# Performance work log

Measured on AMD Instinct MI355X. Metric: run time of the kernel, lower is better.

Reference implementation:

```python
import jax, jax.numpy as jnp
import numpy as np
from jax import lax

B_J0 = 0.01
BETA = 1.8
GAMMA = 0.5
LENS = 0.5
SCALE = 6.0
HIGHT = 0.15


def _gaussian(x, mu, sigma):
    return jnp.exp(-((x - mu) ** 2) / (2.0 * sigma ** 2)) / (jnp.sqrt(2.0 * jnp.pi) * sigma)


@jax.custom_vjp
def spike_fn(v):
    return (v > 0).astype(v.dtype)


def _spike_fwd(v):
    return spike_fn(v), v


def _spike_bwd(v, g):
    temp = (_gaussian(v, 0.0, LENS) * (1.0 + HIGHT)
            - _gaussian(v, LENS, SCALE * LENS) * HIGHT
            - _gaussian(v, -LENS, SCALE * LENS) * HIGHT)
    return (g * temp * GAMMA,)


spike_fn.defvjp(_spike_fwd, _spike_bwd)


def setup_inputs() -> dict:
    key = jax.random.key(0)
    ks = jax.random.split(key, 8)
    S, B, D, H = 1024, 2048, 2, 128
    x = jax.random.normal(ks[0], (S, B, D), dtype=jnp.float32)
    y = jax.random.normal(ks[1], (B,), dtype=jnp.float32)
    z = jnp.zeros((B, H), dtype=jnp.float32)

    def lin_init(k, out_f, in_f):
        bound = 1.0 / np.sqrt(in_f)
        return jax.random.uniform(k, (out_f, in_f), jnp.float32, -bound, bound)

    W1x = lin_init(ks[2], H, D + H)
    WtauM = lin_init(ks[3], H, 2 * H)
    WtauAdp = lin_init(ks[4], H, 2 * H)
    # readout uses xavier_normal_
    Wlin = jax.random.normal(ks[5], (1, H), jnp.float32) * np.sqrt(2.0 / (1 + H))
    return {
        'x': x, 'y': y,
        'h0_mem': z, 'h0_spk': z, 'h0_b': z,
        'W1x': W1x, 'b1x': jnp.zeros((H,), jnp.float32),
        'WtauM': WtauM, 'btauM': jnp.zeros((H,), jnp.float32),
        'WtauAdp': WtauAdp, 'btauAdp': jnp.zeros((H,), jnp.float32),
        'Wlin': Wlin, 'blin': jnp.zeros((1,), jnp.float32),
    }


def reference(x, y, h0_mem, h0_spk, h0_b, W1x, b1x, WtauM, btauM, WtauAdp, btauAdp, Wlin, blin):
    def step(carry, x_t):
        mem, spk, bb = carry
        dense = jnp.concatenate([x_t, spk], axis=-1) @ W1x.T + b1x          # [B,H]
        tauM = jax.nn.sigmoid(jnp.concatenate([dense, mem], axis=-1) @ WtauM.T + btauM)
        tauA = jax.nn.sigmoid(jnp.concatenate([dense, bb], axis=-1) @ WtauAdp.T + btauAdp)
        bb = tauA * bb + (1.0 - tauA) * spk
        Bth = B_J0 + BETA * bb
        mem = mem * tauM + (1.0 - tauM) * dense - Bth * spk
        spk = spike_fn(mem - Bth)
        return (mem, spk, bb), None

    (mem, spk, bb), _ = lax.scan(step, (h0_mem, h0_spk, h0_b), x)
    out = (mem @ Wlin.T + blin)[:, 0]                                       # [B]
    loss = jnp.mean((out - y) ** 2)
    return loss
```

## Files before the change

### kernel.cpp

```cpp
#include <hip/hip_runtime.h>
#include <math.h>

#define S_LEN 1024
#define BATCH 2048
#define MTILE 8
#define HID   128
#define NBLK  (BATCH / MTILE)
#define INV2048 (1.0f / 2048.0f)

#define H_M1H 0
#define H_M1L 20480
#define H_MSH 40960
#define H_MSL 61440
#define H_ASH 81920
#define H_ASL 102400
#define H_WMH 122880
#define H_WML 139264
#define H_WBH 155648
#define H_WBL 172032
#define OFF_PART_F 94208

typedef _Float16 half8 __attribute__((ext_vector_type(8)));
typedef _Float16 half4 __attribute__((ext_vector_type(4)));
typedef float floatx4 __attribute__((ext_vector_type(4)));

#define MFMA(a, b, c) __builtin_amdgcn_mfma_f32_16x16x32_f16((a), (b), (c), 0, 0, 0)

__device__ __forceinline__ void put_hl(_Float16* ws, int hiBase, int loBase,
                                       int idx, float v) {
  _Float16 hi = (_Float16)v;
  ws[hiBase + idx] = hi;
  ws[loBase + idx] = (_Float16)((v - (float)hi) * 2048.0f);
}

__device__ __forceinline__ float dpp_xor8(float v) {
  int sw = __builtin_amdgcn_update_dpp(0, __float_as_int(v),
                                       0x128 , 0xF, 0xF, true);
  return __int_as_float(sw);
}

__global__ __launch_bounds__(192) void prep(
    const float* __restrict__ W1x, const float* __restrict__ b1x,
    const float* __restrict__ WtauM, const float* __restrict__ btauM,
    const float* __restrict__ WtauAdp, const float* __restrict__ btauAdp,
    _Float16* __restrict__ ws) {
  const int h = blockIdx.x, k = threadIdx.x;
  if (k >= 160) return;
  if (k < 128) {
    float w1 = W1x[h * 130 + 2 + k];
    float s1 = 0.f, s2 = 0.f;
    for (int d = 0; d < 128; ++d) {
      float wd = W1x[d * 130 + 2 + k];
      s1 += WtauM[h * 256 + d] * wd;
      s2 += WtauAdp[h * 256 + d] * wd;
    }
    put_hl(ws, H_M1H, H_M1L, h * 160 + k, w1);
    put_hl(ws, H_MSH, H_MSL, h * 160 + k, s1);
    put_hl(ws, H_ASH, H_ASL, h * 160 + k, s2);
    put_hl(ws, H_WMH, H_WML, h * 128 + k, WtauM[h * 256 + 128 + k]);
    put_hl(ws, H_WBH, H_WBL, h * 128 + k, WtauAdp[h * 256 + 128 + k]);
  } else if (k < 131) {
    const int col = k - 128;
    float m1v = (col == 0) ? b1x[h] : W1x[h * 130 + (col - 1)];
    float sm = 0.f, sa = 0.f;
    for (int d = 0; d < 128; ++d) {
      float cv = (col == 0) ? b1x[d] : W1x[d * 130 + (col - 1)];
      sm += WtauM[h * 256 + d] * cv;
      sa += WtauAdp[h * 256 + d] * cv;
    }
    if (col == 0) { sm += btauM[h]; sa += btauAdp[h]; }
    put_hl(ws, H_M1H, H_M1L, h * 160 + k, m1v);
    put_hl(ws, H_MSH, H_MSL, h * 160 + k, sm);
    put_hl(ws, H_ASH, H_ASL, h * 160 + k, sa);
  } else {
    put_hl(ws, H_M1H, H_M1L, h * 160 + k, 0.f);
    put_hl(ws, H_MSH, H_MSL, h * 160 + k, 0.f);
    put_hl(ws, H_ASH, H_ASL, h * 160 + k, 0.f);
  }
}

struct SLds {
  _Float16 spk[2][4][256];
  _Float16 zero16[8];
  _Float16 mem[2][4][512];
  _Float16 bbp[2][4][512];
  float red[8][8];
  float red2[8];
};

__global__ __launch_bounds__(512, 2) void snn_main(
    const float* __restrict__ x, const float* __restrict__ y,
    const float* __restrict__ h0m, const float* __restrict__ h0s,
    const float* __restrict__ h0b,
    const float* __restrict__ Wlin, const float* __restrict__ blin,
    const _Float16* __restrict__ W, float* __restrict__ wsout) {
  __shared__ SLds L;

  const int tid  = threadIdx.x;
  const int w    = tid >> 6;
  const int lane = tid & 63;
  const int c    = lane & 15;
  const int q    = lane >> 4;
  const int bbase = blockIdx.x * MTILE;
  const bool act = (c < 8);

  half8 m1h[5], m1l[5], msh[5], msl[5], ash[5], asl[5];
  half8 wmh[4], wml[4], wbh[4], wbl[4];
  {
    const int hA = w * 16 + c;
#pragma unroll
    for (int f = 0; f < 5; ++f) {
      const int o = hA * 160 + f * 32 + q * 8;
      m1h[f] = *(const half8*)&W[H_M1H + o];
      m1l[f] = *(const half8*)&W[H_M1L + o];
      msh[f] = *(const half8*)&W[H_MSH + o];
      msl[f] = *(const half8*)&W[H_MSL + o];
      ash[f] = *(const half8*)&W[H_ASH + o];
      asl[f] = *(const half8*)&W[H_ASL + o];
    }
#pragma unroll
    for (int f = 0; f < 4; ++f) {
      const int o = hA * 128 + f * 32 + q * 8;
      wmh[f] = *(const half8*)&W[H_WMH + o];
      wml[f] = *(const half8*)&W[H_WML + o];
      wbh[f] = *(const half8*)&W[H_WBH + o];
      wbl[f] = *(const half8*)&W[H_WBL + o];
    }
  }

  if (tid == 0) {
    *(half8*)&L.zero16[0] = half8{0, 0, 0, 0, 0, 0, 0, 0};
  }

  float memv[4], spk[4], bb[4];
#pragma unroll
  for (int r = 0; r < 4; ++r) { memv[r] = 0.f; spk[r] = 0.f; bb[r] = 0.f; }
  if (act) {
#pragma unroll
    for (int r = 0; r < 4; ++r) {
      const int gi = (bbase + c) * HID + w * 16 + q * 4 + r;
      memv[r] = h0m[gi]; spk[r] = h0s[gi]; bb[r] = h0b[gi];
    }
  }

  const int fW  = w >> 1;
  const int qp  = (w & 1) * 2 + (q >> 1);
  const int wiH = (qp * 16 + c) * 8 + (q & 1) * 4;
  const int wiL = wiH + 64;
  const int wiS = (qp * 8 + c) * 8 + (q & 1) * 4;
  const int ri  = lane * 8;
  const _Float16* spkB0 = act ? &L.spk[0][0][(q * 8 + c) * 8] : L.zero16;
  const _Float16* spkB1 = act ? &L.spk[1][0][(q * 8 + c) * 8] : L.zero16;
  const int spkStep = act ? 256 : 0;

  if (act) {
    half4 ps, mh4, ml4, bh4, bl4;
#pragma unroll
    for (int r = 0; r < 4; ++r) {
      ps[r] = (_Float16)spk[r];
      float v = memv[r]; _Float16 hi = (_Float16)v;
      mh4[r] = hi; ml4[r] = (_Float16)((v - (float)hi) * 2048.0f);
      v = bb[r]; hi = (_Float16)v;
      bh4[r] = hi; bl4[r] = (_Float16)((v - (float)hi) * 2048.0f);
    }
    *(half4*)&L.spk[0][fW][wiS] = ps;
    *(half4*)&L.mem[0][fW][wiH] = mh4; *(half4*)&L.mem[0][fW][wiL] = ml4;
    *(half4*)&L.bbp[0][fW][wiH] = bh4; *(half4*)&L.bbp[0][fW][wiL] = bl4;
  }
  __syncthreads();

  const float* xb = x + (size_t)(bbase + (c & 7)) * 2;
  float2 xv = *(const float2*)xb;
  const _Float16 e0c = act ? (_Float16)1.0f : (_Float16)0.0f;

#pragma unroll 1
  for (int t = 0; t < S_LEN; ++t) {
    const int p = t & 1, pn = p ^ 1;
    const size_t tn = (t + 1 < S_LEN) ? (size_t)(t + 1) : (size_t)t;
    float2 xnx = *(const float2*)(xb + tn * (size_t)(BATCH * 2));

    half8 E;
    {
      _Float16 xh0 = (_Float16)xv.x, xh1 = (_Float16)xv.y;
      _Float16 xl0 = (_Float16)((xv.x - (float)xh0) * 2048.0f);
      _Float16 xl1 = (_Float16)((xv.y - (float)xh1) * 2048.0f);
      E = half8{e0c, act ? xh0 : xl0, act ? xh1 : xl1, 0, 0, 0, 0, 0};
    }

    const _Float16* sB = p ? spkB1 : spkB0;

    floatx4 d1 = {0.f,0.f,0.f,0.f}, d2 = {0.f,0.f,0.f,0.f};
    floatx4 m1 = {0.f,0.f,0.f,0.f}, m2 = {0.f,0.f,0.f,0.f};
    floatx4 a1 = {0.f,0.f,0.f,0.f}, a2 = {0.f,0.f,0.f,0.f};

#pragma unroll
    for (int f = 0; f < 4; ++f) {
      half8 S = *(const half8*)&sB[f * spkStep];
      half8 M = *(const half8*)&L.mem[p][f][ri];
      half8 B = *(const half8*)&L.bbp[p][f][ri];
      d1 = MFMA(m1h[f], S, d1);
      d2 = MFMA(m1l[f], S, d2);
      m1 = MFMA(msh[f], S, m1);
      m1 = MFMA(wmh[f], M, m1);
      m2 = MFMA(msl[f], S, m2);
      m2 = MFMA(wml[f], M, m2);
      a1 = MFMA(ash[f], S, a1);
      a1 = MFMA(wbh[f], B, a1);
      a2 = MFMA(asl[f], S, a2);
      a2 = MFMA(wbl[f], B, a2);
    }
    {
      d1 = MFMA(m1h[4], E, d1);
      d2 = MFMA(m1l[4], E, d2);
      m1 = MFMA(msh[4], E, m1);
      m2 = MFMA(msl[4], E, m2);
      a1 = MFMA(ash[4], E, a1);
      a2 = MFMA(asl[4], E, a2);
    }

#pragma unroll
    for (int r = 0; r < 4; ++r) {
      d2[r] += dpp_xor8(d1[r]);
      m2[r] += dpp_xor8(m1[r]);
      a2[r] += dpp_xor8(a1[r]);
    }

    half4 ps, mh4, ml4, bh4, bl4;
#pragma unroll
    for (int r = 0; r < 4; ++r) {
      float den  = d1[r] + d2[r] * INV2048;
      float preM = m1[r] + m2[r] * INV2048;
      float preA = a1[r] + a2[r] * INV2048;
      float tM = __builtin_amdgcn_rcpf(1.0f + __expf(-preM));
      float tA = __builtin_amdgcn_rcpf(1.0f + __expf(-preA));
      bb[r] = tA * bb[r] + (1.0f - tA) * spk[r];
      float Bth = 0.01f + 1.8f * bb[r];
      memv[r] = memv[r] * tM + (1.0f - tM) * den - Bth * spk[r];
      spk[r] = (memv[r] - Bth) > 0.0f ? 1.0f : 0.0f;
      ps[r] = (_Float16)spk[r];
      float v = memv[r]; _Float16 hi = (_Float16)v;
      mh4[r] = hi; ml4[r] = (_Float16)((v - (float)hi) * 2048.0f);
      v = bb[r]; hi = (_Float16)v;
      bh4[r] = hi; bl4[r] = (_Float16)((v - (float)hi) * 2048.0f);
    }
    if (act) {
      *(half4*)&L.spk[pn][fW][wiS] = ps;
      *(half4*)&L.mem[pn][fW][wiH] = mh4; *(half4*)&L.mem[pn][fW][wiL] = ml4;
      *(half4*)&L.bbp[pn][fW][wiH] = bh4; *(half4*)&L.bbp[pn][fW][wiL] = bl4;
    }
    xv = xnx;
    __syncthreads();
  }

  float part = 0.0f;
#pragma unroll
  for (int r = 0; r < 4; ++r)
    part += memv[r] * Wlin[w * 16 + q * 4 + r];
  part += __shfl_xor(part, 16);
  part += __shfl_xor(part, 32);
  if (lane < 8) L.red[w][c] = part;
  __syncthreads();
  if (tid < 8) {
    float s = 0.0f;
#pragma unroll
    for (int ww = 0; ww < 8; ++ww) s += L.red[ww][tid];
    float out = s + blin[0];
    float d = out - y[bbase + tid];
    L.red2[tid] = d * d;
  }
  __syncthreads();
  if (tid == 0) {
    float s = 0.0f;
#pragma unroll
    for (int m = 0; m < MTILE; ++m) s += L.red2[m];
    wsout[blockIdx.x] = s;
  }
}

__global__ __launch_bounds__(256) void final_reduce(const float* __restrict__ part,
                                                    float* __restrict__ out) {
  __shared__ float sh[256];
  int t = threadIdx.x;
  sh[t] = part[t];
  __syncthreads();
  for (int s = 128; s > 0; s >>= 1) {
    if (t < s) sh[t] += sh[t + s];
    __syncthreads();
  }
  if (t == 0) out[0] = sh[0] * (1.0f / (float)BATCH);
}

extern "C" void kernel_launch(void* const* d_in, const int* in_sizes, int n_in,
                              void* d_out, int out_size, void* d_ws, size_t ws_size,
                              hipStream_t stream) {
  const float* x       = (const float*)d_in[0];
  const float* y       = (const float*)d_in[1];
  const float* h0m     = (const float*)d_in[2];
  const float* h0s     = (const float*)d_in[3];
  const float* h0b     = (const float*)d_in[4];
  const float* W1x     = (const float*)d_in[5];
  const float* b1x     = (const float*)d_in[6];
  const float* WtauM   = (const float*)d_in[7];
  const float* btauM   = (const float*)d_in[8];
  const float* WtauAdp = (const float*)d_in[9];
  const float* btauAdp = (const float*)d_in[10];
  const float* Wlin    = (const float*)d_in[11];
  const float* blin    = (const float*)d_in[12];
  _Float16* wsf16 = (_Float16*)d_ws;
  float* wspart = (float*)d_ws + OFF_PART_F;

  prep<<<128, 192, 0, stream>>>(W1x, b1x, WtauM, btauM, WtauAdp, btauAdp, wsf16);
  snn_main<<<NBLK, 512, 0, stream>>>(x, y, h0m, h0s, h0b, Wlin, blin,
                                     wsf16, wspart);
  final_reduce<<<1, 256, 0, stream>>>(wspart, (float*)d_out);
}
```

Measured before the change: 1.757 ms.

## Use all 16 MFMA columns for batch rows instead of hi/lo split lanes

Doubles the batch tile per block from 8 to 16 rows so every MFMA column carries a real batch element. The fp16 hi/lo compensation moves from lane halves (combined via DPP) to separate hi and lo LDS buffers plus extra MFMA accumulators. The negative log2(e) factor is folded into the precomputed tau weights so the sigmoid uses exp2 directly. This halves the block count to 128 with one block per CU and adds two MFMAs per k-slice, trading occupancy and extra matrix work for removing wasted columns and DPP shuffles.

```diff
diff --git a/kernel.cpp b/kernel.cpp
--- a/kernel.cpp
+++ b/kernel.cpp
@@ -3,10 +3,11 @@
 
 #define S_LEN 1024
 #define BATCH 2048
-#define MTILE 8
+#define MTILE 16
 #define HID   128
 #define NBLK  (BATCH / MTILE)
 #define INV2048 (1.0f / 2048.0f)
+#define NLOG2E (-1.44269504088896341f)
 
 #define H_M1H 0
 #define H_M1L 20480
@@ -31,12 +32,6 @@
   _Float16 hi = (_Float16)v;
   ws[hiBase + idx] = hi;
   ws[loBase + idx] = (_Float16)((v - (float)hi) * 2048.0f);
-}
-
-__device__ __forceinline__ float dpp_xor8(float v) {
-  int sw = __builtin_amdgcn_update_dpp(0, __float_as_int(v),
-                                       0x128 , 0xF, 0xF, true);
-  return __int_as_float(sw);
 }
 
 __global__ __launch_bounds__(192) void prep(
@@ -55,12 +50,12 @@
       s2 += WtauAdp[h * 256 + d] * wd;
     }
     put_hl(ws, H_M1H, H_M1L, h * 160 + k, w1);
-    put_hl(ws, H_MSH, H_MSL, h * 160 + k, s1);
-    put_hl(ws, H_ASH, H_ASL, h * 160 + k, s2);
-    put_hl(ws, H_WMH, H_WML, h * 128 + k, WtauM[h * 256 + 128 + k]);
-    put_hl(ws, H_WBH, H_WBL, h * 128 + k, WtauAdp[h * 256 + 128 + k]);
-  } else if (k < 131) {
-    const int col = k - 128;
+    put_hl(ws, H_MSH, H_MSL, h * 160 + k, s1 * NLOG2E);
+    put_hl(ws, H_ASH, H_ASL, h * 160 + k, s2 * NLOG2E);
+    put_hl(ws, H_WMH, H_WML, h * 128 + k, WtauM[h * 256 + 128 + k] * NLOG2E);
+    put_hl(ws, H_WBH, H_WBL, h * 128 + k, WtauAdp[h * 256 + 128 + k] * NLOG2E);
+  } else if (k < 133) {
+    const int col = (k == 128) ? 0 : ((k == 129 || k == 131) ? 1 : 2);
     float m1v = (col == 0) ? b1x[h] : W1x[h * 130 + (col - 1)];
     float sm = 0.f, sa = 0.f;
     for (int d = 0; d < 128; ++d) {
@@ -69,26 +64,36 @@
       sa += WtauAdp[h * 256 + d] * cv;
     }
     if (col == 0) { sm += btauM[h]; sa += btauAdp[h]; }
-    put_hl(ws, H_M1H, H_M1L, h * 160 + k, m1v);
-    put_hl(ws, H_MSH, H_MSL, h * 160 + k, sm);
-    put_hl(ws, H_ASH, H_ASL, h * 160 + k, sa);
+    sm *= NLOG2E; sa *= NLOG2E;
+    const int idx = h * 160 + k;
+    if (k < 131) {
+      put_hl(ws, H_M1H, H_M1L, idx, m1v);
+      put_hl(ws, H_MSH, H_MSL, idx, sm);
+      put_hl(ws, H_ASH, H_ASL, idx, sa);
+    } else {
+      ws[H_M1H + idx] = (_Float16)0.0f; ws[H_M1L + idx] = (_Float16)m1v;
+      ws[H_MSH + idx] = (_Float16)0.0f; ws[H_MSL + idx] = (_Float16)sm;
+      ws[H_ASH + idx] = (_Float16)0.0f; ws[H_ASL + idx] = (_Float16)sa;
+    }
   } else {
-    put_hl(ws, H_M1H, H_M1L, h * 160 + k, 0.f);
-    put_hl(ws, H_MSH, H_MSL, h * 160 + k, 0.f);
-    put_hl(ws, H_ASH, H_ASL, h * 160 + k, 0.f);
+    const int idx = h * 160 + k;
+    ws[H_M1H + idx] = 0; ws[H_M1L + idx] = 0;
+    ws[H_MSH + idx] = 0; ws[H_MSL + idx] = 0;
+    ws[H_ASH + idx] = 0; ws[H_ASL + idx] = 0;
   }
 }
 
 struct SLds {
-  _Float16 spk[2][4][256];
-  _Float16 zero16[8];
-  _Float16 mem[2][4][512];
-  _Float16 bbp[2][4][512];
-  float red[8][8];
-  float red2[8];
+  _Float16 spk[2][4][512];
+  _Float16 memh[2][4][512];
+  _Float16 meml[2][4][512];
+  _Float16 bbph[2][4][512];
+  _Float16 bbpl[2][4][512];
+  float red[8][16];
+  float red2[16];
 };
 
-__global__ __launch_bounds__(512, 2) void snn_main(
+__global__ __launch_bounds__(512, 1) void snn_main(
     const float* __restrict__ x, const float* __restrict__ y,
     const float* __restrict__ h0m, const float* __restrict__ h0s,
     const float* __restrict__ h0b,
@@ -97,17 +102,16 @@
   __shared__ SLds L;
 
   const int tid  = threadIdx.x;
-  const int w    = tid >> 6;
+  const int wg   = tid >> 6;
   const int lane = tid & 63;
   const int c    = lane & 15;
   const int q    = lane >> 4;
   const int bbase = blockIdx.x * MTILE;
-  const bool act = (c < 8);
 
   half8 m1h[5], m1l[5], msh[5], msl[5], ash[5], asl[5];
   half8 wmh[4], wml[4], wbh[4], wbl[4];
   {
-    const int hA = w * 16 + c;
+    const int hA = wg * 16 + c;
 #pragma unroll
     for (int f = 0; f < 5; ++f) {
       const int o = hA * 160 + f * 32 + q * 8;
@@ -128,50 +132,44 @@
     }
   }
 
-  if (tid == 0) {
-    *(half8*)&L.zero16[0] = half8{0, 0, 0, 0, 0, 0, 0, 0};
-  }
-
-  float memv[4], spk[4], bb[4];
-#pragma unroll
-  for (int r = 0; r < 4; ++r) { memv[r] = 0.f; spk[r] = 0.f; bb[r] = 0.f; }
-  if (act) {
+  const int h0i = wg * 16 + q * 4;
+  float memv[4], spk4[4], bb[4];
+  {
+    const int gi = (bbase + c) * HID + h0i;
+    float4 tm = *(const float4*)&h0m[gi];
+    float4 ts = *(const float4*)&h0s[gi];
+    float4 tb = *(const float4*)&h0b[gi];
+    memv[0] = tm.x; memv[1] = tm.y; memv[2] = tm.z; memv[3] = tm.w;
+    spk4[0] = ts.x; spk4[1] = ts.y; spk4[2] = ts.z; spk4[3] = ts.w;
+    bb[0]   = tb.x; bb[1]   = tb.y; bb[2]   = tb.z; bb[3]   = tb.w;
+  }
+
+  const int fW = wg >> 1;
+  const int qp = (wg & 1) * 2 + (q >> 1);
+  const int wi = (qp * 16 + c) * 8 + (q & 1) * 4;
+  const int ri = lane * 8;
+
+  {
+    half4 ps, mh4, ml4, bh4, bl4;
 #pragma unroll
     for (int r = 0; r < 4; ++r) {
-      const int gi = (bbase + c) * HID + w * 16 + q * 4 + r;
-      memv[r] = h0m[gi]; spk[r] = h0s[gi]; bb[r] = h0b[gi];
-    }
-  }
-
-  const int fW  = w >> 1;
-  const int qp  = (w & 1) * 2 + (q >> 1);
-  const int wiH = (qp * 16 + c) * 8 + (q & 1) * 4;
-  const int wiL = wiH + 64;
-  const int wiS = (qp * 8 + c) * 8 + (q & 1) * 4;
-  const int ri  = lane * 8;
-  const _Float16* spkB0 = act ? &L.spk[0][0][(q * 8 + c) * 8] : L.zero16;
-  const _Float16* spkB1 = act ? &L.spk[1][0][(q * 8 + c) * 8] : L.zero16;
-  const int spkStep = act ? 256 : 0;
-
-  if (act) {
-    half4 ps, mh4, ml4, bh4, bl4;
-#pragma unroll
-    for (int r = 0; r < 4; ++r) {
-      ps[r] = (_Float16)spk[r];
+      ps[r] = (_Float16)spk4[r];
       float v = memv[r]; _Float16 hi = (_Float16)v;
       mh4[r] = hi; ml4[r] = (_Float16)((v - (float)hi) * 2048.0f);
       v = bb[r]; hi = (_Float16)v;
       bh4[r] = hi; bl4[r] = (_Float16)((v - (float)hi) * 2048.0f);
     }
-    *(half4*)&L.spk[0][fW][wiS] = ps;
-    *(half4*)&L.mem[0][fW][wiH] = mh4; *(half4*)&L.mem[0][fW][wiL] = ml4;
-    *(half4*)&L.bbp[0][fW][wiH] = bh4; *(half4*)&L.bbp[0][fW][wiL] = bl4;
+    *(half4*)&L.spk[0][fW][wi]  = ps;
+    *(half4*)&L.memh[0][fW][wi] = mh4; *(half4*)&L.meml[0][fW][wi] = ml4;
+    *(half4*)&L.bbph[0][fW][wi] = bh4; *(half4*)&L.bbpl[0][fW][wi] = bl4;
   }
   __syncthreads();
 
-  const float* xb = x + (size_t)(bbase + (c & 7)) * 2;
+  const float qm = (q == 0) ? 1.0f : 0.0f;
+  const _Float16 e0 = (q == 0) ? (_Float16)1.0f : (_Float16)0.0f;
+
+  const float* xb = x + (size_t)(bbase + c) * 2;
   float2 xv = *(const float2*)xb;
-  const _Float16 e0c = act ? (_Float16)1.0f : (_Float16)0.0f;
 
 #pragma unroll 1
   for (int t = 0; t < S_LEN; ++t) {
@@ -181,86 +179,79 @@
 
     half8 E;
     {
-      _Float16 xh0 = (_Float16)xv.x, xh1 = (_Float16)xv.y;
-      _Float16 xl0 = (_Float16)((xv.x - (float)xh0) * 2048.0f);
-      _Float16 xl1 = (_Float16)((xv.y - (float)xh1) * 2048.0f);
-      E = half8{e0c, act ? xh0 : xl0, act ? xh1 : xl1, 0, 0, 0, 0, 0};
-    }
-
-    const _Float16* sB = p ? spkB1 : spkB0;
-
-    floatx4 d1 = {0.f,0.f,0.f,0.f}, d2 = {0.f,0.f,0.f,0.f};
-    floatx4 m1 = {0.f,0.f,0.f,0.f}, m2 = {0.f,0.f,0.f,0.f};
-    floatx4 a1 = {0.f,0.f,0.f,0.f}, a2 = {0.f,0.f,0.f,0.f};
+      float xe0 = xv.x * qm, xe1 = xv.y * qm;
+      _Float16 xh0 = (_Float16)xe0, xh1 = (_Float16)xe1;
+      _Float16 xl0 = (_Float16)((xe0 - (float)xh0) * 2048.0f);
+      _Float16 xl1 = (_Float16)((xe1 - (float)xh1) * 2048.0f);
+      E = half8{e0, xh0, xh1, xl0, xl1, 0, 0, 0};
+    }
+
+    floatx4 d1 = {0,0,0,0}, d2 = {0,0,0,0};
+    floatx4 mA1 = {0,0,0,0}, mA2 = {0,0,0,0}, mA3 = {0,0,0,0};
+    floatx4 aA1 = {0,0,0,0}, aA2 = {0,0,0,0}, aA3 = {0,0,0,0};
 
 #pragma unroll
     for (int f = 0; f < 4; ++f) {
-      half8 S = *(const half8*)&sB[f * spkStep];
-      half8 M = *(const half8*)&L.mem[p][f][ri];
-      half8 B = *(const half8*)&L.bbp[p][f][ri];
-      d1 = MFMA(m1h[f], S, d1);
-      d2 = MFMA(m1l[f], S, d2);
-      m1 = MFMA(msh[f], S, m1);
-      m1 = MFMA(wmh[f], M, m1);
-      m2 = MFMA(msl[f], S, m2);
-      m2 = MFMA(wml[f], M, m2);
-      a1 = MFMA(ash[f], S, a1);
-      a1 = MFMA(wbh[f], B, a1);
-      a2 = MFMA(asl[f], S, a2);
-      a2 = MFMA(wbl[f], B, a2);
+      half8 S  = *(const half8*)&L.spk[p][f][ri];
+      half8 Mh = *(const half8*)&L.memh[p][f][ri];
+      half8 Ml = *(const half8*)&L.meml[p][f][ri];
+      half8 Bh = *(const half8*)&L.bbph[p][f][ri];
+      half8 Bl = *(const half8*)&L.bbpl[p][f][ri];
+      d1  = MFMA(m1h[f], S,  d1);
+      d2  = MFMA(m1l[f], S,  d2);
+      mA1 = MFMA(msh[f], S,  mA1);
+      mA1 = MFMA(wmh[f], Mh, mA1);
+      mA2 = MFMA(msl[f], S,  mA2);
+      mA2 = MFMA(wml[f], Mh, mA2);
+      mA3 = MFMA(wmh[f], Ml, mA3);
+      aA1 = MFMA(ash[f], S,  aA1);
+      aA1 = MFMA(wbh[f], Bh, aA1);
+      aA2 = MFMA(asl[f], S,  aA2);
+      aA2 = MFMA(wbl[f], Bh, aA2);
+      aA3 = MFMA(wbh[f], Bl, aA3);
     }
     {
-      d1 = MFMA(m1h[4], E, d1);
-      d2 = MFMA(m1l[4], E, d2);
-      m1 = MFMA(msh[4], E, m1);
-      m2 = MFMA(msl[4], E, m2);
-      a1 = MFMA(ash[4], E, a1);
-      a2 = MFMA(asl[4], E, a2);
-    }
-
+      d1  = MFMA(m1h[4], E, d1);
+      d2  = MFMA(m1l[4], E, d2);
+      mA1 = MFMA(msh[4], E, mA1);
+      mA2 = MFMA(msl[4], E, mA2);
+      aA1 = MFMA(ash[4], E, aA1);
+      aA2 = MFMA(asl[4], E, aA2);
+    }
+
+    half4 ps, mh4, ml4, bh4, bl4;
 #pragma unroll
     for (int r = 0; r < 4; ++r) {
-      d2[r] += dpp_xor8(d1[r]);
-      m2[r] += dpp_xor8(m1[r]);
-      a2[r] += dpp_xor8(a1[r]);
-    }
-
-    half4 ps, mh4, ml4, bh4, bl4;
-#pragma unroll
-    for (int r = 0; r < 4; ++r) {
-      float den  = d1[r] + d2[r] * INV2048;
-      float preM = m1[r] + m2[r] * INV2048;
-      float preA = a1[r] + a2[r] * INV2048;
-      float tM = __builtin_amdgcn_rcpf(1.0f + __expf(-preM));
-      float tA = __builtin_amdgcn_rcpf(1.0f + __expf(-preA));
-      bb[r] = tA * bb[r] + (1.0f - tA) * spk[r];
+      float dv = d1[r] + d2[r] * INV2048;
+      float pM = mA1[r] + (mA2[r] + mA3[r]) * INV2048;
+      float pA = aA1[r] + (aA2[r] + aA3[r]) * INV2048;
+      float tM = __builtin_amdgcn_rcpf(1.0f + __builtin_amdgcn_exp2f(pM));
+      float tA = __builtin_amdgcn_rcpf(1.0f + __builtin_amdgcn_exp2f(pA));
+      bb[r] = tA * bb[r] + (1.0f - tA) * spk4[r];
       float Bth = 0.01f + 1.8f * bb[r];
-      memv[r] = memv[r] * tM + (1.0f - tM) * den - Bth * spk[r];
-      spk[r] = (memv[r] - Bth) > 0.0f ? 1.0f : 0.0f;
-      ps[r] = (_Float16)spk[r];
-      float v = memv[r]; _Float16 hi = (_Float16)v;
+      memv[r] = memv[r] * tM + (1.0f - tM) * dv - Bth * spk4[r];
+      spk4[r] = (memv[r] - Bth) > 0.0f ? 1.0f : 0.0f;
+      ps[r] = (_Float16)spk4[r];
+      float v = bb[r]; _Float16 hi = (_Float16)v;
+      bh4[r] = hi; bl4[r] = (_Float16)((v - (float)hi) * 2048.0f);
+      v = memv[r]; hi = (_Float16)v;
       mh4[r] = hi; ml4[r] = (_Float16)((v - (float)hi) * 2048.0f);
-      v = bb[r]; hi = (_Float16)v;
-      bh4[r] = hi; bl4[r] = (_Float16)((v - (float)hi) * 2048.0f);
-    }
-    if (act) {
-      *(half4*)&L.spk[pn][fW][wiS] = ps;
-      *(half4*)&L.mem[pn][fW][wiH] = mh4; *(half4*)&L.mem[pn][fW][wiL] = ml4;
-      *(half4*)&L.bbp[pn][fW][wiH] = bh4; *(half4*)&L.bbp[pn][fW][wiL] = bl4;
-    }
+    }
+    *(half4*)&L.bbph[pn][fW][wi] = bh4; *(half4*)&L.bbpl[pn][fW][wi] = bl4;
+    *(half4*)&L.spk[pn][fW][wi]  = ps;
+    *(half4*)&L.memh[pn][fW][wi] = mh4; *(half4*)&L.meml[pn][fW][wi] = ml4;
+
     xv = xnx;
     __syncthreads();
   }
 
-  float part = 0.0f;
-#pragma unroll
-  for (int r = 0; r < 4; ++r)
-    part += memv[r] * Wlin[w * 16 + q * 4 + r];
+  float part = memv[0] * Wlin[h0i] + memv[1] * Wlin[h0i + 1]
+             + memv[2] * Wlin[h0i + 2] + memv[3] * Wlin[h0i + 3];
   part += __shfl_xor(part, 16);
   part += __shfl_xor(part, 32);
-  if (lane < 8) L.red[w][c] = part;
+  if (lane < 16) L.red[wg][c] = part;
   __syncthreads();
-  if (tid < 8) {
+  if (tid < 16) {
     float s = 0.0f;
 #pragma unroll
     for (int ww = 0; ww < 8; ++ww) s += L.red[ww][tid];
@@ -277,13 +268,13 @@
   }
 }
 
-__global__ __launch_bounds__(256) void final_reduce(const float* __restrict__ part,
+__global__ __launch_bounds__(128) void final_reduce(const float* __restrict__ part,
                                                     float* __restrict__ out) {
-  __shared__ float sh[256];
+  __shared__ float sh[128];
   int t = threadIdx.x;
   sh[t] = part[t];
   __syncthreads();
-  for (int s = 128; s > 0; s >>= 1) {
+  for (int s = 64; s > 0; s >>= 1) {
     if (t < s) sh[t] += sh[t + s];
     __syncthreads();
   }
@@ -312,5 +303,5 @@
   prep<<<128, 192, 0, stream>>>(W1x, b1x, WtauM, btauM, WtauAdp, btauAdp, wsf16);
   snn_main<<<NBLK, 512, 0, stream>>>(x, y, h0m, h0s, h0b, Wlin, blin,
                                      wsf16, wspart);
-  final_reduce<<<1, 256, 0, stream>>>(wspart, (float*)d_out);
-}
+  final_reduce<<<1, 128, 0, stream>>>(wspart, (float*)d_out);
+}
```

Measured after the change: 2.965 ms. 68.8% more time.
